# Performance work log

Measured on AMD Instinct MI355X. Metric: run time of the kernel, lower is better.

Reference implementation:

```python
import jax, jax.numpy as jnp
import numpy as np

C = 512
H = 8

def setup_inputs() -> dict:
    key = jax.random.key(0)
    ks = jax.random.split(key, 5)
    x = jax.random.normal(ks[0], (4, C, 2048), dtype=jnp.float32)
    # Conv1d(kernel_size=1) == pointwise linear: weight [out, in], bias [out]
    qkv_w = jax.random.normal(ks[1], (3 * C, C), dtype=jnp.float32) * (1.0 / np.sqrt(C))
    qkv_b = jax.random.normal(ks[2], (3 * C,), dtype=jnp.float32) * 0.02
    proj_w = jax.random.normal(ks[3], (C, C), dtype=jnp.float32) * (1.0 / np.sqrt(C))
    proj_b = jax.random.normal(ks[4], (C,), dtype=jnp.float32) * 0.02
    return {"x": x, "qkv_w": qkv_w, "qkv_b": qkv_b, "proj_w": proj_w, "proj_b": proj_b}

def reference(x, qkv_w, qkv_b, proj_w, proj_b):
    b, c, t = x.shape
    scale = c ** (-0.5)  # NOTE: full channel count, matching the torch module
    # pointwise conv: [3C, C] @ [b, C, T] -> [b, 3C, T]
    qkv = jnp.einsum('oc,bct->bot', qkv_w, x) + qkv_b[None, :, None]
    q, k, v = jnp.split(qkv, 3, axis=1)
    d = c // H
    q = q.reshape(b, H, d, t)
    k = k.reshape(b, H, d, t)
    v = v.reshape(b, H, d, t)
    attn = jnp.einsum('bhct,bhcs->bhts', q, k) * scale
    attn = jax.nn.softmax(attn, axis=-1)
    out = jnp.einsum('bhts,bhcs->bhct', attn, v)
    out = out.reshape(b, c, t)
    out = jnp.einsum('oc,bct->bot', proj_w, out) + proj_b[None, :, None]
    return x + out
```

## Files before the change

kernel.cpp:

```cpp
#include <hip/hip_runtime.h>
#include <hip/hip_bf16.h>
#include <math.h>

#define B_DIM 4
#define C_DIM 512
#define T_DIM 2048
#define H_DIM 8
#define OC3   1536
#define VN_STRIDE 2064
#define SCALE 0.044194173824159216f
#define SCALE2 (0.044194173824159216f * 1.4426950408889634f)

typedef unsigned short ushortT;
typedef unsigned int uintT;
typedef __attribute__((ext_vector_type(8))) short bf16x8;
typedef __attribute__((ext_vector_type(4))) short bf16x4;
typedef __attribute__((ext_vector_type(4))) float f32x4;

__device__ __forceinline__ ushortT f2bf(float f) {
    union { float f; uintT u; } v; v.f = f;
    uintT r = v.u + 0x7FFF + ((v.u >> 16) & 1);
    return (ushortT)(r >> 16);
}
__device__ __forceinline__ float bf2f(ushortT h) {
    union { uintT u; float f; } v; v.u = ((uintT)h) << 16;
    return v.f;
}
__device__ __forceinline__ uintT pack2bf(float a, float b) {
    uintT ua = __float_as_uint(a) + 0x8000u;
    uintT ub = __float_as_uint(b) + 0x8000u;
    return (ua >> 16) | (ub & 0xFFFF0000u);
}

__global__ __launch_bounds__(256) void conv_w(const float* __restrict__ qw,
                                              const float* __restrict__ pw,
                                              ushortT* __restrict__ qwb,
                                              ushortT* __restrict__ pwb) {
    int i = blockIdx.x * 256 + threadIdx.x;
    int idx = i * 4;
    if (idx < OC3 * C_DIM) {
        float4 v = *(const float4*)(qw + idx);
        qwb[idx + 0] = f2bf(v.x); qwb[idx + 1] = f2bf(v.y);
        qwb[idx + 2] = f2bf(v.z); qwb[idx + 3] = f2bf(v.w);
    } else {
        idx -= OC3 * C_DIM;
        float4 v = *(const float4*)(pw + idx);
        pwb[idx + 0] = f2bf(v.x); pwb[idx + 1] = f2bf(v.y);
        pwb[idx + 2] = f2bf(v.z); pwb[idx + 3] = f2bf(v.w);
    }
}

__global__ __launch_bounds__(256) void conv_x(const float* __restrict__ x,
                                              ushortT* __restrict__ xb) {
    __shared__ float xs[64][65];
    const int b = blockIdx.z, c0 = blockIdx.y * 64, t0 = blockIdx.x * 64;
    const int tid = threadIdx.x;
    #pragma unroll
    for (int it = 0; it < 4; ++it) {
        int idx = it * 256 + tid;
        int r = idx >> 4, ch = idx & 15;
        float4 v = *(const float4*)(x + ((size_t)(b * C_DIM + c0 + r)) * T_DIM + t0 + ch * 4);
        xs[r][ch * 4 + 0] = v.x; xs[r][ch * 4 + 1] = v.y;
        xs[r][ch * 4 + 2] = v.z; xs[r][ch * 4 + 3] = v.w;
    }
    __syncthreads();
    #pragma unroll
    for (int it = 0; it < 2; ++it) {
        int idx = it * 256 + tid;
        int rt = idx >> 3, ch = idx & 7;
        union { ushortT s[8]; uint4 v; } tmp;
        #pragma unroll
        for (int k = 0; k < 8; ++k) tmp.s[k] = f2bf(xs[ch * 8 + k][rt]);
        *(uint4*)(xb + ((size_t)b * T_DIM + t0 + rt) * C_DIM + c0 + ch * 8) = tmp.v;
    }
}

__global__ __launch_bounds__(256, 2) void gemm_qkv(const ushortT* __restrict__ A,
                                                   const ushortT* __restrict__ Bw,
                                                   const float* __restrict__ bias,
                                                   ushortT* __restrict__ out,
                                                   ushortT* __restrict__ Vn) {
    __shared__ ushortT As[4096], Bs[4096];
    const int tid = threadIdx.x, lane = tid & 63, wid = tid >> 6;
    const int u = lane & 15, q = lane >> 4;
    const int wm = wid & 1, wn = wid >> 1;
    const int m0 = blockIdx.x * 128, n0 = blockIdx.y * 128;
    const int arow = tid >> 1, acs = (tid & 1) * 2;
    const int swz = (arow >> 1) & 3;

    f32x4 acc[4][4];
    const f32x4 z = {0.f, 0.f, 0.f, 0.f};
    #pragma unroll
    for (int mi = 0; mi < 4; ++mi)
        #pragma unroll
        for (int ni = 0; ni < 4; ++ni) acc[mi][ni] = z;

    for (int k0 = 0; k0 < 512; k0 += 32) {
        uint4 av0 = *(const uint4*)(A  + (size_t)(m0 + arow) * 512 + k0 + acs * 8);
        uint4 av1 = *(const uint4*)(A  + (size_t)(m0 + arow) * 512 + k0 + acs * 8 + 8);
        uint4 bv0 = *(const uint4*)(Bw + (size_t)(n0 + arow) * 512 + k0 + acs * 8);
        uint4 bv1 = *(const uint4*)(Bw + (size_t)(n0 + arow) * 512 + k0 + acs * 8 + 8);
        __syncthreads();
        *(uint4*)&As[arow * 32 + (((acs + 0) ^ swz) << 3)] = av0;
        *(uint4*)&As[arow * 32 + (((acs + 1) ^ swz) << 3)] = av1;
        *(uint4*)&Bs[arow * 32 + (((acs + 0) ^ swz) << 3)] = bv0;
        *(uint4*)&Bs[arow * 32 + (((acs + 1) ^ swz) << 3)] = bv1;
        __syncthreads();
        const int rswz = (q ^ ((u >> 1) & 3)) << 3;
        bf16x8 af[4], bfr[4];
        #pragma unroll
        for (int mi = 0; mi < 4; ++mi)
            af[mi] = *(const bf16x8*)&As[(wm * 64 + mi * 16 + u) * 32 + rswz];
        #pragma unroll
        for (int ni = 0; ni < 4; ++ni)
            bfr[ni] = *(const bf16x8*)&Bs[(wn * 64 + ni * 16 + u) * 32 + rswz];
        #pragma unroll
        for (int mi = 0; mi < 4; ++mi)
            #pragma unroll
            for (int ni = 0; ni < 4; ++ni)
                acc[mi][ni] = __builtin_amdgcn_mfma_f32_16x16x32_bf16(
                    af[mi], bfr[ni], acc[mi][ni], 0, 0, 0);
    }
    if (n0 < 1024) {
        const float scl = (n0 < 512) ? SCALE2 : 1.0f;
        #pragma unroll
        for (int ni = 0; ni < 4; ++ni) {
            int o = n0 + wn * 64 + ni * 16 + u;
            float bv = bias[o];
            #pragma unroll
            for (int mi = 0; mi < 4; ++mi)
                #pragma unroll
                for (int r = 0; r < 4; ++r) {
                    int m = m0 + wm * 64 + mi * 16 + q * 4 + r;
                    out[(size_t)m * OC3 + o] = f2bf((acc[mi][ni][r] + bv) * scl);
                }
        }
    } else {
        #pragma unroll
        for (int ni = 0; ni < 4; ++ni) {
            int o = n0 + wn * 64 + ni * 16 + u;
            float bv = bias[o];
            int oo = o - 1024;
            int hv = oo >> 6, d = oo & 63;
            #pragma unroll
            for (int mi = 0; mi < 4; ++mi) {
                int m = m0 + wm * 64 + mi * 16 + q * 4;
                int b = m >> 11, t = m & 2047;
                uint2 w;
                w.x = pack2bf(acc[mi][ni][0] + bv, acc[mi][ni][1] + bv);
                w.y = pack2bf(acc[mi][ni][2] + bv, acc[mi][ni][3] + bv);
                *(uint2*)(Vn + ((size_t)((b * 8 + hv) * 64 + d)) * VN_STRIDE + t) = w;
            }
        }
    }
}

__global__ __launch_bounds__(256, 2)
void flash(const ushortT* __restrict__ qkvT, const ushortT* __restrict__ Vn,
           ushortT* __restrict__ AO)
{
    __shared__ __align__(16) ushortT lds[4 * 4608];
    __shared__ float Lbuf[4][64];

    const int tid = threadIdx.x, lane = tid & 63, wid = tid >> 6;
    const int u = lane & 15, q = lane >> 4;
    const int gid = blockIdx.y * 32 + blockIdx.x;
    const int xg = gid >> 3;
    const int bh = (gid & 7) * 4 + (xg >> 5);
    const int tb = xg & 31;
    const int bb = bh >> 3, h = bh & 7;
    const int tblk = tb * 64;
    const size_t qbase = (size_t)bb * T_DIM * OC3;

    bf16x8 qb[4][2];
    #pragma unroll
    for (int ti = 0; ti < 4; ++ti)
        #pragma unroll
        for (int kst = 0; kst < 2; ++kst)
            qb[ti][kst] = *(const bf16x8*)(qkvT + qbase
                + (size_t)(tblk + ti * 16 + u) * OC3 + h * 64 + kst * 32 + q * 8);

    const ushortT* kp[4];
    #pragma unroll
    for (int si = 0; si < 4; ++si)
        kp[si] = qkvT + qbase + (size_t)(wid * 512 + si * 16 + u) * OC3 + 512 + h * 64;
    const ushortT* vp[4];
    #pragma unroll
    for (int ci = 0; ci < 4; ++ci)
        vp[ci] = Vn + ((size_t)bh * 64 + ci * 16 + u) * VN_STRIDE + wid * 512 + q * 4;

    f32x4 acc[4][4];
    const f32x4 z = {0.f, 0.f, 0.f, 0.f};
    #pragma unroll
    for (int ci = 0; ci < 4; ++ci)
        #pragma unroll
        for (int ti = 0; ti < 4; ++ti) acc[ci][ti] = z;
    float lpart[4] = {0.f, 0.f, 0.f, 0.f};

    for (int rnd = 0; rnd < 8; ++rnd) {
        bf16x8 ka[4][2];
        #pragma unroll
        for (int si = 0; si < 4; ++si) {
            ka[si][0] = *(const bf16x8*)(kp[si] + q * 8);
            ka[si][1] = *(const bf16x8*)(kp[si] + 32 + q * 8);
        }
        bf16x4 va[4][4];
        #pragma unroll
        for (int si = 0; si < 4; ++si)
            #pragma unroll
            for (int ci = 0; ci < 4; ++ci)
                va[si][ci] = *(const bf16x4*)(vp[ci] + si * 16);

        #pragma unroll
        for (int si = 0; si < 4; ++si) {
            f32x4 sacc[4] = {z, z, z, z};
            #pragma unroll
            for (int ti = 0; ti < 4; ++ti)
                sacc[ti] = __builtin_amdgcn_mfma_f32_16x16x32_bf16(
                    ka[si][0], qb[ti][0], sacc[ti], 0, 0, 0);
            #pragma unroll
            for (int ti = 0; ti < 4; ++ti)
                sacc[ti] = __builtin_amdgcn_mfma_f32_16x16x32_bf16(
                    ka[si][1], qb[ti][1], sacc[ti], 0, 0, 0);
            #pragma unroll
            for (int ti = 0; ti < 4; ++ti) {
                float p0 = __builtin_amdgcn_exp2f(sacc[ti][0]);
                float p1 = __builtin_amdgcn_exp2f(sacc[ti][1]);
                float p2 = __builtin_amdgcn_exp2f(sacc[ti][2]);
                float p3 = __builtin_amdgcn_exp2f(sacc[ti][3]);
                lpart[ti] += (p0 + p1) + (p2 + p3);
                union { uint2 u2; bf16x4 v; } pw;
                pw.u2.x = pack2bf(p0, p1);
                pw.u2.y = pack2bf(p2, p3);
                #pragma unroll
                for (int ci = 0; ci < 4; ++ci)
                    acc[ci][ti] = __builtin_amdgcn_mfma_f32_16x16x16bf16_1k(
                        va[si][ci], pw.v, acc[ci][ti], 0, 0, 0);
            }
        }
        #pragma unroll
        for (int si = 0; si < 4; ++si) kp[si] += 64 * OC3;
        #pragma unroll
        for (int ci = 0; ci < 4; ++ci) vp[ci] += 64;
    }

    #pragma unroll
    for (int ti = 0; ti < 4; ++ti) {
        float l = lpart[ti];
        l += __shfl_xor(l, 16);
        l += __shfl_xor(l, 32);
        lpart[ti] = l;
    }
    ushortT* Ob = lds + wid * 4608;
    if (q == 0) {
        #pragma unroll
        for (int ti = 0; ti < 4; ++ti) Lbuf[wid][ti * 16 + u] = lpart[ti];
    }
    #pragma unroll
    for (int ci = 0; ci < 4; ++ci)
        #pragma unroll
        for (int ti = 0; ti < 4; ++ti) {
            uint2 w;
            w.x = pack2bf(acc[ci][ti][0], acc[ci][ti][1]);
            w.y = pack2bf(acc[ci][ti][2], acc[ci][ti][3]);
            *(uint2*)&Ob[(ti * 16 + u) * 72 + ci * 16 + q * 4] = w;
        }
    __syncthreads();
    {
        const int t = tid >> 2, cs = (tid & 3) * 16;
        float linv = 1.0f / (Lbuf[0][t] + Lbuf[1][t] + Lbuf[2][t] + Lbuf[3][t]);
        float vs[16];
        #pragma unroll
        for (int j = 0; j < 16; ++j) vs[j] = 0.f;
        #pragma unroll
        for (int w = 0; w < 4; ++w) {
            const ushortT* row = lds + w * 4608 + t * 72 + cs;
            #pragma unroll
            for (int j2 = 0; j2 < 2; ++j2) {
                uint4 rv = *(const uint4*)(row + j2 * 8);
                const uintT* rp = (const uintT*)&rv;
                #pragma unroll
                for (int k = 0; k < 4; ++k) {
                    vs[j2 * 8 + k * 2 + 0] += bf2f((ushortT)(rp[k] & 0xFFFF));
                    vs[j2 * 8 + k * 2 + 1] += bf2f((ushortT)(rp[k] >> 16));
                }
            }
        }
        uint4 o0, o1;
        uintT* op0 = (uintT*)&o0; uintT* op1 = (uintT*)&o1;
        #pragma unroll
        for (int k = 0; k < 4; ++k) {
            op0[k] = pack2bf(vs[k * 2] * linv, vs[k * 2 + 1] * linv);
            op1[k] = pack2bf(vs[8 + k * 2] * linv, vs[8 + k * 2 + 1] * linv);
        }
        size_t orow = ((size_t)bb * T_DIM + tblk + t) * C_DIM + h * 64 + cs;
        *(uint4*)(AO + orow) = o0;
        *(uint4*)(AO + orow + 8) = o1;
    }
}

__global__ __launch_bounds__(256, 2) void gemm_proj(const ushortT* __restrict__ Wp,
                                                    const ushortT* __restrict__ AOv,
                                                    const float* __restrict__ bias,
                                                    const float* __restrict__ xres,
                                                    float* __restrict__ out) {
    __shared__ ushortT As[4096], Bs[4096];
    const int tid = threadIdx.x, lane = tid & 63, wid = tid >> 6;
    const int u = lane & 15, q = lane >> 4;
    const int wm = wid & 1, wn = wid >> 1;
    const int m0 = blockIdx.y * 128, n0 = blockIdx.x * 128;
    const int arow = tid >> 1, acs = (tid & 1) * 2;
    const int swz = (arow >> 1) & 3;

    f32x4 acc[4][4];
    const f32x4 z = {0.f, 0.f, 0.f, 0.f};
    #pragma unroll
    for (int mi = 0; mi < 4; ++mi)
        #pragma unroll
        for (int ni = 0; ni < 4; ++ni) acc[mi][ni] = z;

    for (int k0 = 0; k0 < 512; k0 += 32) {
        uint4 av0 = *(const uint4*)(Wp  + (size_t)(m0 + arow) * 512 + k0 + acs * 8);
        uint4 av1 = *(const uint4*)(Wp  + (size_t)(m0 + arow) * 512 + k0 + acs * 8 + 8);
        uint4 bv0 = *(const uint4*)(AOv + (size_t)(n0 + arow) * 512 + k0 + acs * 8);
        uint4 bv1 = *(const uint4*)(AOv + (size_t)(n0 + arow) * 512 + k0 + acs * 8 + 8);
        __syncthreads();
        *(uint4*)&As[arow * 32 + (((acs + 0) ^ swz) << 3)] = av0;
        *(uint4*)&As[arow * 32 + (((acs + 1) ^ swz) << 3)] = av1;
        *(uint4*)&Bs[arow * 32 + (((acs + 0) ^ swz) << 3)] = bv0;
        *(uint4*)&Bs[arow * 32 + (((acs + 1) ^ swz) << 3)] = bv1;
        __syncthreads();
        const int rswz = (q ^ ((u >> 1) & 3)) << 3;
        bf16x8 af[4], bfr[4];
        #pragma unroll
        for (int mi = 0; mi < 4; ++mi)
            af[mi] = *(const bf16x8*)&As[(wm * 64 + mi * 16 + u) * 32 + rswz];
        #pragma unroll
        for (int ni = 0; ni < 4; ++ni)
            bfr[ni] = *(const bf16x8*)&Bs[(wn * 64 + ni * 16 + u) * 32 + rswz];
        #pragma unroll
        for (int mi = 0; mi < 4; ++mi)
            #pragma unroll
            for (int ni = 0; ni < 4; ++ni)
                acc[mi][ni] = __builtin_amdgcn_mfma_f32_16x16x32_bf16(
                    af[mi], bfr[ni], acc[mi][ni], 0, 0, 0);
    }
    #pragma unroll
    for (int mi = 0; mi < 4; ++mi)
        #pragma unroll
        for (int r = 0; r < 4; ++r) {
            int o = m0 + wm * 64 + mi * 16 + q * 4 + r;
            float bv = bias[o];
            #pragma unroll
            for (int ni = 0; ni < 4; ++ni) {
                int n = n0 + wn * 64 + ni * 16 + u;
                int b = n >> 11, t = n & 2047;
                size_t oi = ((size_t)b * C_DIM + o) * T_DIM + t;
                out[oi] = acc[mi][ni][r] + bv + xres[oi];
            }
        }
}

extern "C" void kernel_launch(void* const* d_in, const int* in_sizes, int n_in,
                              void* d_out, int out_size, void* d_ws, size_t ws_size,
                              hipStream_t stream)
{
    const float* x      = (const float*)d_in[0];
    const float* qkv_w  = (const float*)d_in[1];
    const float* qkv_b  = (const float*)d_in[2];
    const float* proj_w = (const float*)d_in[3];
    const float* proj_b = (const float*)d_in[4];
    float* out = (float*)d_out;

    char* ws = (char*)d_ws;
    ushortT* xb   = (ushortT*)(ws);
    ushortT* wqb  = (ushortT*)(ws +  8388608);
    ushortT* wpb  = (ushortT*)(ws +  9961472);
    ushortT* qkvT = (ushortT*)(ws + 10485760);
    ushortT* Vn   = (ushortT*)(ws + 35651584);
    ushortT* AO   = (ushortT*)(ws + 44105728);

    conv_w   <<<1024, 256, 0, stream>>>(qkv_w, proj_w, wqb, wpb);
    conv_x   <<<dim3(32, 8, 4), 256, 0, stream>>>(x, xb);
    gemm_qkv <<<dim3(64, 12),   256, 0, stream>>>(xb, wqb, qkv_b, qkvT, Vn);
    flash    <<<dim3(32, 32),   256, 0, stream>>>(qkvT, Vn, AO);
    gemm_proj<<<dim3(64, 4),    256, 0, stream>>>(wpb, AO, proj_b, x, out);
}
```

Before: 184.3 us.

## Merge weight and input conversion kernels; software-pipeline K/V loads in flash loop

```diff
diff --git a/kernel.cpp b/kernel.cpp
--- a/kernel.cpp
+++ b/kernel.cpp
@@ -32,29 +32,31 @@
     return (ua >> 16) | (ub & 0xFFFF0000u);
 }
 
-__global__ __launch_bounds__(256) void conv_w(const float* __restrict__ qw,
-                                              const float* __restrict__ pw,
-                                              ushortT* __restrict__ qwb,
-                                              ushortT* __restrict__ pwb) {
-    int i = blockIdx.x * 256 + threadIdx.x;
-    int idx = i * 4;
-    if (idx < OC3 * C_DIM) {
-        float4 v = *(const float4*)(qw + idx);
-        qwb[idx + 0] = f2bf(v.x); qwb[idx + 1] = f2bf(v.y);
-        qwb[idx + 2] = f2bf(v.z); qwb[idx + 3] = f2bf(v.w);
-    } else {
-        idx -= OC3 * C_DIM;
-        float4 v = *(const float4*)(pw + idx);
-        pwb[idx + 0] = f2bf(v.x); pwb[idx + 1] = f2bf(v.y);
-        pwb[idx + 2] = f2bf(v.z); pwb[idx + 3] = f2bf(v.w);
-    }
-}
-
-__global__ __launch_bounds__(256) void conv_x(const float* __restrict__ x,
-                                              ushortT* __restrict__ xb) {
+__global__ __launch_bounds__(256) void prep(const float* __restrict__ x,
+                                            const float* __restrict__ qw,
+                                            const float* __restrict__ pw,
+                                            ushortT* __restrict__ xb,
+                                            ushortT* __restrict__ qwb,
+                                            ushortT* __restrict__ pwb) {
     __shared__ float xs[64][65];
-    const int b = blockIdx.z, c0 = blockIdx.y * 64, t0 = blockIdx.x * 64;
     const int tid = threadIdx.x;
+    const int blk = blockIdx.x;
+    if (blk >= 1024) {
+        int idx = ((blk - 1024) * 256 + tid) * 4;
+        if (idx < OC3 * C_DIM) {
+            float4 v = *(const float4*)(qw + idx);
+            qwb[idx + 0] = f2bf(v.x); qwb[idx + 1] = f2bf(v.y);
+            qwb[idx + 2] = f2bf(v.z); qwb[idx + 3] = f2bf(v.w);
+        } else {
+            idx -= OC3 * C_DIM;
+            float4 v = *(const float4*)(pw + idx);
+            pwb[idx + 0] = f2bf(v.x); pwb[idx + 1] = f2bf(v.y);
+            pwb[idx + 2] = f2bf(v.z); pwb[idx + 3] = f2bf(v.w);
+        }
+        return;
+    }
+    const int b = blk >> 8, rem = blk & 255;
+    const int c0 = (rem >> 5) * 64, t0 = (rem & 31) * 64;
     #pragma unroll
     for (int it = 0; it < 4; ++it) {
         int idx = it * 256 + tid;
@@ -197,51 +199,71 @@
         for (int ti = 0; ti < 4; ++ti) acc[ci][ti] = z;
     float lpart[4] = {0.f, 0.f, 0.f, 0.f};
 
+    bf16x8 ka[4][2];
+    bf16x4 va[4][4];
+    #pragma unroll
+    for (int si = 0; si < 4; ++si) {
+        ka[si][0] = *(const bf16x8*)(kp[si] + q * 8);
+        ka[si][1] = *(const bf16x8*)(kp[si] + 32 + q * 8);
+    }
+    #pragma unroll
+    for (int si = 0; si < 4; ++si)
+        #pragma unroll
+        for (int ci = 0; ci < 4; ++ci)
+            va[si][ci] = *(const bf16x4*)(vp[ci] + si * 16);
+
+    #pragma unroll
     for (int rnd = 0; rnd < 8; ++rnd) {
-        bf16x8 ka[4][2];
+        f32x4 sacc[4][4];
         #pragma unroll
         for (int si = 0; si < 4; ++si) {
-            ka[si][0] = *(const bf16x8*)(kp[si] + q * 8);
-            ka[si][1] = *(const bf16x8*)(kp[si] + 32 + q * 8);
-        }
-        bf16x4 va[4][4];
+            #pragma unroll
+            for (int ti = 0; ti < 4; ++ti)
+                sacc[si][ti] = __builtin_amdgcn_mfma_f32_16x16x32_bf16(
+                    ka[si][0], qb[ti][0], z, 0, 0, 0);
+            #pragma unroll
+            for (int ti = 0; ti < 4; ++ti)
+                sacc[si][ti] = __builtin_amdgcn_mfma_f32_16x16x32_bf16(
+                    ka[si][1], qb[ti][1], sacc[si][ti], 0, 0, 0);
+        }
+        if (rnd < 7) {
+            #pragma unroll
+            for (int si = 0; si < 4; ++si) {
+                kp[si] += 64 * OC3;
+                ka[si][0] = *(const bf16x8*)(kp[si] + q * 8);
+                ka[si][1] = *(const bf16x8*)(kp[si] + 32 + q * 8);
+            }
+        }
+        union { uint2 u2; bf16x4 v; } pv[4][4];
         #pragma unroll
         for (int si = 0; si < 4; ++si)
             #pragma unroll
-            for (int ci = 0; ci < 4; ++ci)
-                va[si][ci] = *(const bf16x4*)(vp[ci] + si * 16);
-
-        #pragma unroll
-        for (int si = 0; si < 4; ++si) {
-            f32x4 sacc[4] = {z, z, z, z};
+            for (int ti = 0; ti < 4; ++ti) {
+                float p0 = __builtin_amdgcn_exp2f(sacc[si][ti][0]);
+                float p1 = __builtin_amdgcn_exp2f(sacc[si][ti][1]);
+                float p2 = __builtin_amdgcn_exp2f(sacc[si][ti][2]);
+                float p3 = __builtin_amdgcn_exp2f(sacc[si][ti][3]);
+                lpart[ti] += (p0 + p1) + (p2 + p3);
+                pv[si][ti].u2.x = pack2bf(p0, p1);
+                pv[si][ti].u2.y = pack2bf(p2, p3);
+            }
+        #pragma unroll
+        for (int si = 0; si < 4; ++si)
             #pragma unroll
             for (int ti = 0; ti < 4; ++ti)
-                sacc[ti] = __builtin_amdgcn_mfma_f32_16x16x32_bf16(
-                    ka[si][0], qb[ti][0], sacc[ti], 0, 0, 0);
-            #pragma unroll
-            for (int ti = 0; ti < 4; ++ti)
-                sacc[ti] = __builtin_amdgcn_mfma_f32_16x16x32_bf16(
-                    ka[si][1], qb[ti][1], sacc[ti], 0, 0, 0);
-            #pragma unroll
-            for (int ti = 0; ti < 4; ++ti) {
-                float p0 = __builtin_amdgcn_exp2f(sacc[ti][0]);
-                float p1 = __builtin_amdgcn_exp2f(sacc[ti][1]);
-                float p2 = __builtin_amdgcn_exp2f(sacc[ti][2]);
-                float p3 = __builtin_amdgcn_exp2f(sacc[ti][3]);
-                lpart[ti] += (p0 + p1) + (p2 + p3);
-                union { uint2 u2; bf16x4 v; } pw;
-                pw.u2.x = pack2bf(p0, p1);
-                pw.u2.y = pack2bf(p2, p3);
                 #pragma unroll
                 for (int ci = 0; ci < 4; ++ci)
                     acc[ci][ti] = __builtin_amdgcn_mfma_f32_16x16x16bf16_1k(
-                        va[si][ci], pw.v, acc[ci][ti], 0, 0, 0);
-            }
-        }
-        #pragma unroll
-        for (int si = 0; si < 4; ++si) kp[si] += 64 * OC3;
-        #pragma unroll
-        for (int ci = 0; ci < 4; ++ci) vp[ci] += 64;
+                        va[si][ci], pv[si][ti].v, acc[ci][ti], 0, 0, 0);
+        if (rnd < 7) {
+            #pragma unroll
+            for (int ci = 0; ci < 4; ++ci) vp[ci] += 64;
+            #pragma unroll
+            for (int si = 0; si < 4; ++si)
+                #pragma unroll
+                for (int ci = 0; ci < 4; ++ci)
+                    va[si][ci] = *(const bf16x4*)(vp[ci] + si * 16);
+        }
     }
 
     #pragma unroll
@@ -380,8 +402,7 @@
     ushortT* Vn   = (ushortT*)(ws + 35651584);
     ushortT* AO   = (ushortT*)(ws + 44105728);
 
-    conv_w   <<<1024, 256, 0, stream>>>(qkv_w, proj_w, wqb, wpb);
-    conv_x   <<<dim3(32, 8, 4), 256, 0, stream>>>(x, xb);
+    prep     <<<2048, 256, 0, stream>>>(x, qkv_w, proj_w, xb, wqb, wpb);
     gemm_qkv <<<dim3(64, 12),   256, 0, stream>>>(xb, wqb, qkv_b, qkvT, Vn);
     flash    <<<dim3(32, 32),   256, 0, stream>>>(qkvT, Vn, AO);
     gemm_proj<<<dim3(64, 4),    256, 0, stream>>>(wpb, AO, proj_b, x, out);
```

Result: no change. 184.9 us (+0.3%).

## Pad intermediate buffer strides and merge conversion kernels into one prep launch

Applied to the files above, without the earlier changes.

```diff
diff --git a/kernel.cpp b/kernel.cpp
--- a/kernel.cpp
+++ b/kernel.cpp
@@ -7,7 +7,11 @@
 #define T_DIM 2048
 #define H_DIM 8
 #define OC3   1536
-#define VN_STRIDE 2064
+#define QKV_STRIDE 1664
+#define VN_STRIDE  2176
+#define XB_STRIDE   544
+#define W_STRIDE    544
+#define AO_STRIDE   544
 #define SCALE 0.044194173824159216f
 #define SCALE2 (0.044194173824159216f * 1.4426950408889634f)
 
@@ -32,29 +36,33 @@
     return (ua >> 16) | (ub & 0xFFFF0000u);
 }
 
-__global__ __launch_bounds__(256) void conv_w(const float* __restrict__ qw,
-                                              const float* __restrict__ pw,
-                                              ushortT* __restrict__ qwb,
-                                              ushortT* __restrict__ pwb) {
-    int i = blockIdx.x * 256 + threadIdx.x;
-    int idx = i * 4;
-    if (idx < OC3 * C_DIM) {
-        float4 v = *(const float4*)(qw + idx);
-        qwb[idx + 0] = f2bf(v.x); qwb[idx + 1] = f2bf(v.y);
-        qwb[idx + 2] = f2bf(v.z); qwb[idx + 3] = f2bf(v.w);
-    } else {
-        idx -= OC3 * C_DIM;
-        float4 v = *(const float4*)(pw + idx);
-        pwb[idx + 0] = f2bf(v.x); pwb[idx + 1] = f2bf(v.y);
-        pwb[idx + 2] = f2bf(v.z); pwb[idx + 3] = f2bf(v.w);
-    }
-}
-
-__global__ __launch_bounds__(256) void conv_x(const float* __restrict__ x,
-                                              ushortT* __restrict__ xb) {
+__global__ __launch_bounds__(256) void prep(const float* __restrict__ x,
+                                            const float* __restrict__ qw,
+                                            const float* __restrict__ pw,
+                                            ushortT* __restrict__ xb,
+                                            ushortT* __restrict__ qwb,
+                                            ushortT* __restrict__ pwb) {
     __shared__ float xs[64][65];
-    const int b = blockIdx.z, c0 = blockIdx.y * 64, t0 = blockIdx.x * 64;
     const int tid = threadIdx.x;
+    const int blk = blockIdx.x;
+    if (blk >= 1024) {
+        int idx = ((blk - 1024) * 256 + tid) * 4;
+        if (idx < OC3 * C_DIM) {
+            int row = idx >> 9, col = idx & 511;
+            float4 v = *(const float4*)(qw + idx);
+            ushortT* d = qwb + row * W_STRIDE + col;
+            d[0] = f2bf(v.x); d[1] = f2bf(v.y); d[2] = f2bf(v.z); d[3] = f2bf(v.w);
+        } else {
+            idx -= OC3 * C_DIM;
+            int row = idx >> 9, col = idx & 511;
+            float4 v = *(const float4*)(pw + idx);
+            ushortT* d = pwb + row * W_STRIDE + col;
+            d[0] = f2bf(v.x); d[1] = f2bf(v.y); d[2] = f2bf(v.z); d[3] = f2bf(v.w);
+        }
+        return;
+    }
+    const int b = blk >> 8, rem = blk & 255;
+    const int c0 = (rem >> 5) * 64, t0 = (rem & 31) * 64;
     #pragma unroll
     for (int it = 0; it < 4; ++it) {
         int idx = it * 256 + tid;
@@ -71,7 +79,7 @@
         union { ushortT s[8]; uint4 v; } tmp;
         #pragma unroll
         for (int k = 0; k < 8; ++k) tmp.s[k] = f2bf(xs[ch * 8 + k][rt]);
-        *(uint4*)(xb + ((size_t)b * T_DIM + t0 + rt) * C_DIM + c0 + ch * 8) = tmp.v;
+        *(uint4*)(xb + ((size_t)b * T_DIM + t0 + rt) * XB_STRIDE + c0 + ch * 8) = tmp.v;
     }
 }
 
@@ -96,10 +104,10 @@
         for (int ni = 0; ni < 4; ++ni) acc[mi][ni] = z;
 
     for (int k0 = 0; k0 < 512; k0 += 32) {
-        uint4 av0 = *(const uint4*)(A  + (size_t)(m0 + arow) * 512 + k0 + acs * 8);
-        uint4 av1 = *(const uint4*)(A  + (size_t)(m0 + arow) * 512 + k0 + acs * 8 + 8);
-        uint4 bv0 = *(const uint4*)(Bw + (size_t)(n0 + arow) * 512 + k0 + acs * 8);
-        uint4 bv1 = *(const uint4*)(Bw + (size_t)(n0 + arow) * 512 + k0 + acs * 8 + 8);
+        uint4 av0 = *(const uint4*)(A  + (size_t)(m0 + arow) * XB_STRIDE + k0 + acs * 8);
+        uint4 av1 = *(const uint4*)(A  + (size_t)(m0 + arow) * XB_STRIDE + k0 + acs * 8 + 8);
+        uint4 bv0 = *(const uint4*)(Bw + (size_t)(n0 + arow) * W_STRIDE + k0 + acs * 8);
+        uint4 bv1 = *(const uint4*)(Bw + (size_t)(n0 + arow) * W_STRIDE + k0 + acs * 8 + 8);
         __syncthreads();
         *(uint4*)&As[arow * 32 + (((acs + 0) ^ swz) << 3)] = av0;
         *(uint4*)&As[arow * 32 + (((acs + 1) ^ swz) << 3)] = av1;
@@ -132,7 +140,7 @@
                 #pragma unroll
                 for (int r = 0; r < 4; ++r) {
                     int m = m0 + wm * 64 + mi * 16 + q * 4 + r;
-                    out[(size_t)m * OC3 + o] = f2bf((acc[mi][ni][r] + bv) * scl);
+                    out[(size_t)m * QKV_STRIDE + o] = f2bf((acc[mi][ni][r] + bv) * scl);
                 }
         }
     } else {
@@ -170,7 +178,7 @@
     const int tb = xg & 31;
     const int bb = bh >> 3, h = bh & 7;
     const int tblk = tb * 64;
-    const size_t qbase = (size_t)bb * T_DIM * OC3;
+    const size_t qbase = (size_t)bb * T_DIM * QKV_STRIDE;
 
     bf16x8 qb[4][2];
     #pragma unroll
@@ -178,12 +186,12 @@
         #pragma unroll
         for (int kst = 0; kst < 2; ++kst)
             qb[ti][kst] = *(const bf16x8*)(qkvT + qbase
-                + (size_t)(tblk + ti * 16 + u) * OC3 + h * 64 + kst * 32 + q * 8);
+                + (size_t)(tblk + ti * 16 + u) * QKV_STRIDE + h * 64 + kst * 32 + q * 8);
 
     const ushortT* kp[4];
     #pragma unroll
     for (int si = 0; si < 4; ++si)
-        kp[si] = qkvT + qbase + (size_t)(wid * 512 + si * 16 + u) * OC3 + 512 + h * 64;
+        kp[si] = qkvT + qbase + (size_t)(wid * 512 + si * 16 + u) * QKV_STRIDE + 512 + h * 64;
     const ushortT* vp[4];
     #pragma unroll
     for (int ci = 0; ci < 4; ++ci)
@@ -239,7 +247,7 @@
             }
         }
         #pragma unroll
-        for (int si = 0; si < 4; ++si) kp[si] += 64 * OC3;
+        for (int si = 0; si < 4; ++si) kp[si] += 64 * QKV_STRIDE;
         #pragma unroll
         for (int ci = 0; ci < 4; ++ci) vp[ci] += 64;
     }
@@ -293,7 +301,7 @@
             op0[k] = pack2bf(vs[k * 2] * linv, vs[k * 2 + 1] * linv);
             op1[k] = pack2bf(vs[8 + k * 2] * linv, vs[8 + k * 2 + 1] * linv);
         }
-        size_t orow = ((size_t)bb * T_DIM + tblk + t) * C_DIM + h * 64 + cs;
+        size_t orow = ((size_t)bb * T_DIM + tblk + t) * AO_STRIDE + h * 64 + cs;
         *(uint4*)(AO + orow) = o0;
         *(uint4*)(AO + orow + 8) = o1;
     }
@@ -320,10 +328,10 @@
         for (int ni = 0; ni < 4; ++ni) acc[mi][ni] = z;
 
     for (int k0 = 0; k0 < 512; k0 += 32) {
-        uint4 av0 = *(const uint4*)(Wp  + (size_t)(m0 + arow) * 512 + k0 + acs * 8);
-        uint4 av1 = *(const uint4*)(Wp  + (size_t)(m0 + arow) * 512 + k0 + acs * 8 + 8);
-        uint4 bv0 = *(const uint4*)(AOv + (size_t)(n0 + arow) * 512 + k0 + acs * 8);
-        uint4 bv1 = *(const uint4*)(AOv + (size_t)(n0 + arow) * 512 + k0 + acs * 8 + 8);
+        uint4 av0 = *(const uint4*)(Wp  + (size_t)(m0 + arow) * W_STRIDE + k0 + acs * 8);
+        uint4 av1 = *(const uint4*)(Wp  + (size_t)(m0 + arow) * W_STRIDE + k0 + acs * 8 + 8);
+        uint4 bv0 = *(const uint4*)(AOv + (size_t)(n0 + arow) * AO_STRIDE + k0 + acs * 8);
+        uint4 bv1 = *(const uint4*)(AOv + (size_t)(n0 + arow) * AO_STRIDE + k0 + acs * 8 + 8);
         __syncthreads();
         *(uint4*)&As[arow * 32 + (((acs + 0) ^ swz) << 3)] = av0;
         *(uint4*)&As[arow * 32 + (((acs + 1) ^ swz) << 3)] = av1;
@@ -374,14 +382,13 @@
 
     char* ws = (char*)d_ws;
     ushortT* xb   = (ushortT*)(ws);
-    ushortT* wqb  = (ushortT*)(ws +  8388608);
-    ushortT* wpb  = (ushortT*)(ws +  9961472);
-    ushortT* qkvT = (ushortT*)(ws + 10485760);
-    ushortT* Vn   = (ushortT*)(ws + 35651584);
-    ushortT* AO   = (ushortT*)(ws + 44105728);
-
-    conv_w   <<<1024, 256, 0, stream>>>(qkv_w, proj_w, wqb, wpb);
-    conv_x   <<<dim3(32, 8, 4), 256, 0, stream>>>(x, xb);
+    ushortT* wqb  = (ushortT*)(ws +  8912896);
+    ushortT* wpb  = (ushortT*)(ws + 10584064);
+    ushortT* qkvT = (ushortT*)(ws + 11141120);
+    ushortT* Vn   = (ushortT*)(ws + 38404096);
+    ushortT* AO   = (ushortT*)(ws + 47316992);
+
+    prep     <<<2048, 256, 0, stream>>>(x, qkv_w, proj_w, xb, wqb, wpb);
     gemm_qkv <<<dim3(64, 12),   256, 0, stream>>>(xb, wqb, qkv_b, qkvT, Vn);
     flash    <<<dim3(32, 32),   256, 0, stream>>>(qkvT, Vn, AO);
     gemm_proj<<<dim3(64, 4),    256, 0, stream>>>(wpb, AO, proj_b, x, out);
```

New measurement: 209.5 us. +13.7%, slower.
